# Kernel tuning notes

Hardware: AMD Instinct MI355X
Metric: run time of the kernel (lower is better)

## Reference

```python
import jax, jax.numpy as jnp
import numpy as np

N, D = 2, 256
M, L, K, DV = 8, 4, 4, 32
LK = L * K
LEVEL_HW = [(96, 96), (48, 48), (24, 24), (12, 12)]
S = sum(h * w for h, w in LEVEL_HW)  # 12240 flattened pyramid tokens
Q = S
OFFSET_SCALE = 0.5  # sampling_offset_scale_factor


def setup_inputs() -> dict:
    ks = jax.random.split(jax.random.key(0), 16)
    def lin(k, din, dout):
        return jax.random.normal(k, (din, dout), jnp.float32) / np.sqrt(din)
    return {
        "queries": jax.random.normal(ks[0], (N, Q, D), jnp.float32),
        "query_geometries": jax.random.uniform(ks[1], (N, Q, 4), jnp.float32, minval=0.1, maxval=0.9),
        "src_values": jax.random.normal(ks[2], (N, S, D), jnp.float32),
        "W_off": lin(ks[3], D, M * LK * 2) * 0.01,
        "b_off": jax.random.normal(ks[4], (M * LK * 2,), jnp.float32),
        "W_attn": lin(ks[5], D, M * LK),
        "b_attn": jnp.zeros((M * LK,), jnp.float32),
        "W_val": lin(ks[6], D, M * DV),
        "b_val": jnp.zeros((M * DV,), jnp.float32),
        "W_out": lin(ks[7], M * DV, D),
        "b_out": jnp.zeros((D,), jnp.float32),
    }


def _bilinear_sample(vmap_l, grid):
    # vmap_l: [B, dv, H, W]; grid: [B, Q, K, 2] in [-1, 1]
    # Matches F.grid_sample(mode='bilinear', align_corners=False, padding_mode='zeros')
    B, dv, H, W = vmap_l.shape
    x = (grid[..., 0] + 1.0) * (W / 2) - 0.5
    y = (grid[..., 1] + 1.0) * (H / 2) - 0.5
    x0 = jnp.floor(x)
    y0 = jnp.floor(y)
    wx = x - x0
    wy = y - y0
    x0i = x0.astype(jnp.int32)
    y0i = y0.astype(jnp.int32)
    vflat = vmap_l.reshape(B, dv, H * W)

    def corner(xi, yi, w):
        valid = (xi >= 0) & (xi < W) & (yi >= 0) & (yi < H)
        idx = jnp.clip(yi, 0, H - 1) * W + jnp.clip(xi, 0, W - 1)
        g = jax.vmap(lambda vf, i: vf[:, i])(vflat, idx)  # [B, dv, Q, K]
        return g * (w * valid)[:, None, :, :]

    return (corner(x0i, y0i, (1 - wx) * (1 - wy))
            + corner(x0i + 1, y0i, wx * (1 - wy))
            + corner(x0i, y0i + 1, (1 - wx) * wy)
            + corner(x0i + 1, y0i + 1, wx * wy))


def msdeform(queries, query_geometries, src_values, W_off, b_off, W_attn, b_attn,
             W_val, b_val, W_out, b_out):
    # attention weights: softmax over the L*K samples of each head
    attn = jax.nn.softmax((queries @ W_attn + b_attn).reshape(N, Q, M, LK), axis=-1)
    # predicted sampling offsets [N, Q, M, LK, 2]
    off = (queries @ W_off + b_off).reshape(N, Q, M, LK, 2)
    xy = query_geometries[..., :2]
    wh = query_geometries[..., 2:]
    scale = wh * (OFFSET_SCALE / K)  # wh * kv_count_per_level_inverse * sampling_offset_max_value
    pos = xy[:, :, None, None, :] + off * scale[:, :, None, None, :]  # normalized [0,1]
    # collapse (batch, head) -> B = N*M, rescale to [-1,1] for grid_sample semantics
    grid = (2.0 * pos - 1.0).transpose(0, 2, 1, 3, 4).reshape(N * M, Q, LK, 2)
    # project values and rebuild the per-level feature maps
    v = (src_values @ W_val + b_val).reshape(N, S, M, DV)
    samples, s = [], 0
    for l, (H, W) in enumerate(LEVEL_HW):
        vl = v[:, s:s + H * W].reshape(N, H, W, M, DV).transpose(0, 3, 4, 1, 2).reshape(N * M, DV, H, W)
        samples.append(_bilinear_sample(vl, grid[:, :, l * K:(l + 1) * K]))  # [N*M, DV, Q, K]
        s += H * W
    sampled = jnp.concatenate(samples, axis=-1)  # [N*M, DV, Q, LK]
    aw = attn.transpose(0, 2, 1, 3).reshape(N * M, 1, Q, LK)
    out = (sampled * aw).sum(-1)  # weighted reduction -> [N*M, DV, Q]
    out = out.reshape(N, M, DV, Q).transpose(0, 3, 1, 2).reshape(N, Q, M * DV)
    return out @ W_out + b_out  # backprojector


def reference(queries, query_geometries, src_values, W_off, b_off, W_attn, b_attn,
              W_val, b_val, W_out, b_out):
    return msdeform(queries, query_geometries, src_values, W_off, b_off, W_attn,
                    b_attn, W_val, b_val, W_out, b_out)
```

## Files before the change

kernel.cpp:

```cpp
#include <hip/hip_runtime.h>
#include <hip/hip_bf16.h>
#include <hip/hip_fp16.h>
#include <cstddef>

#define NB 2
#define QN 12240
#define SN 12240
#define MREAL 24480
#define MPAD  24576
#define MT    192

typedef unsigned short ushortT;
typedef unsigned int uintT;
typedef __bf16 bf16x8 __attribute__((ext_vector_type(8)));
typedef float f32x4 __attribute__((ext_vector_type(4)));

__device__ __forceinline__ ushortT f2bf(float f) {
    uintT u = __float_as_uint(f);
    uintT r = u + 0x7fffu + ((u >> 16) & 1u);
    return (ushortT)(r >> 16);
}
__device__ __forceinline__ float bf_lo(uintT u) {
    return __uint_as_float(u << 16);
}
__device__ __forceinline__ float bf_hi(uintT u) {
    return __uint_as_float(u & 0xffff0000u);
}

__device__ __forceinline__ void async_ld16(const ushortT* g, ushortT* l) {
    __builtin_amdgcn_global_load_lds(
        (const __attribute__((address_space(1))) unsigned int*)g,
        (__attribute__((address_space(3))) unsigned int*)l, 16, 0, 0);
}

__global__ __launch_bounds__(256) void cast_all(
    const float* __restrict__ q, const float* __restrict__ src,
    const float* __restrict__ Wval, const float* __restrict__ Wattn,
    const float* __restrict__ Woff, const float* __restrict__ Wout,
    ushortT* __restrict__ qb, ushortT* __restrict__ sb,
    ushortT* __restrict__ tval, ushortT* __restrict__ tlo,
    ushortT* __restrict__ tout)
{
    int bx = blockIdx.x;
    if (bx < 6120) {
        const int issrc = bx >= 3060;
        const size_t idx = ((size_t)(bx - (issrc ? 3060 : 0)) * 256 + threadIdx.x) * 8;
        const float* in = issrc ? src : q;
        ushortT* out = issrc ? sb : qb;
        const float4 a = *(const float4*)(in + idx);
        const float4 b = *(const float4*)(in + idx + 4);
        uint4 o;
        o.x = (uintT)f2bf(a.x) | ((uintT)f2bf(a.y) << 16);
        o.y = (uintT)f2bf(a.z) | ((uintT)f2bf(a.w) << 16);
        o.z = (uintT)f2bf(b.x) | ((uintT)f2bf(b.y) << 16);
        o.w = (uintT)f2bf(b.z) | ((uintT)f2bf(b.w) << 16);
        *(uint4*)(out + idx) = o;
        return;
    }
    bx -= 6120;
    const float* W; ushortT* T; int n, Nw, trow;
    if (bx < 256)      { W = Wval;  T = tval; n = bx;       Nw = 256; trow = n; }
    else if (bx < 384) { W = Wattn; T = tlo;  n = bx - 256; Nw = 128; trow = n; }
    else if (bx < 640) { W = Woff;  T = tlo;  n = bx - 384; Nw = 256; trow = n + 128; }
    else               { W = Wout;  T = tout; n = bx - 640; Nw = 256; trow = n; }
    const int k = threadIdx.x;
    T[(size_t)trow * 256 + k] = f2bf(W[(size_t)k * Nw + n]);
}

__global__ __launch_bounds__(256) void gemm_vlo(
    const ushortT* __restrict__ q_bf, const ushortT* __restrict__ src_bf,
    const ushortT* __restrict__ wt_val, const ushortT* __restrict__ wt_lo,
    const float* __restrict__ b_val, const float* __restrict__ b_attn,
    const float* __restrict__ b_off,
    ushortT* __restrict__ v_bf, float* __restrict__ lo_ws)
{
    const int z = blockIdx.x >= 2;
    const int col0 = (z ? blockIdx.x - 2 : blockIdx.x) * 128;

    __shared__ __attribute__((aligned(16))) ushortT As[128 * 32];
    __shared__ __attribute__((aligned(16))) ushortT Bs[128 * 32];

    const ushortT* A  = z ? q_bf : src_bf;
    const ushortT* Bt = z ? wt_lo : wt_val;

    const int tid  = threadIdx.x;
    const int wave = tid >> 6;
    const int lane = tid & 63;
    const int row0 = blockIdx.y * 128;
    const int wr = (wave >> 1) * 64;
    const int wc = (wave & 1) * 64;

    f32x4 acc[4][4];
    #pragma unroll
    for (int i = 0; i < 4; i++)
        #pragma unroll
        for (int j = 0; j < 4; j++)
            acc[i][j] = (f32x4)0.f;

    const int srow = (lane >> 2);
    const int sk8  = (lane & 3) * 8;

    for (int k0 = 0; k0 < 256; k0 += 32) {
        #pragma unroll
        for (int j = 0; j < 2; j++) {
            const int r = wave * 32 + j * 16;
            async_ld16(A  + (size_t)(row0 + r + srow) * 256 + k0 + sk8, &As[r * 32]);
            async_ld16(Bt + (size_t)(col0 + r + srow) * 256 + k0 + sk8, &Bs[r * 32]);
        }
        __syncthreads();

        bf16x8 af[4], bfr[4];
        const int mrow = lane & 15;
        const int kq   = (lane >> 4) * 8;
        #pragma unroll
        for (int i = 0; i < 4; i++) {
            af[i]  = *(const bf16x8*)&As[(wr + i * 16 + mrow) * 32 + kq];
            bfr[i] = *(const bf16x8*)&Bs[(wc + i * 16 + mrow) * 32 + kq];
        }
        #pragma unroll
        for (int i = 0; i < 4; i++)
            #pragma unroll
            for (int j = 0; j < 4; j++)
                acc[i][j] = __builtin_amdgcn_mfma_f32_16x16x32_bf16(
                    af[i], bfr[j], acc[i][j], 0, 0, 0);
        __syncthreads();
    }

    const float* bp = z ? ((col0 < 128) ? b_attn : b_off) : b_val;
    const int cofs  = (z && col0 >= 128) ? 128 : 0;

    #pragma unroll
    for (int i = 0; i < 4; i++) {
        const int rbase = row0 + wr + i * 16 + ((lane >> 4) << 2);
        #pragma unroll
        for (int j = 0; j < 4; j++) {
            const int col = col0 + wc + j * 16 + (lane & 15);
            const float bb = bp[col - cofs];
            #pragma unroll
            for (int r = 0; r < 4; r++) {
                const int row = rbase + r;
                if (row < MREAL) {
                    const float val = acc[i][j][r] + bb;
                    if (z) {
                        lo_ws[(size_t)row * 384 + col] = val;
                    } else {
                        const int nn = row / SN;
                        const int s  = row - nn * SN;
                        const int head = col >> 5, ch = col & 31;
                        v_bf[(((size_t)nn * 8 + head) * SN + s) * 32 + ch] = f2bf(val);
                    }
                }
            }
        }
    }
}

__global__ __launch_bounds__(256) void gemm_out(
    const ushortT* __restrict__ A, const ushortT* __restrict__ Bt,
    const float* __restrict__ bias, float* __restrict__ C)
{
    __shared__ __attribute__((aligned(16))) ushortT As[128 * 32];
    __shared__ __attribute__((aligned(16))) ushortT Bs[128 * 32];

    const int tid  = threadIdx.x;
    const int wave = tid >> 6;
    const int lane = tid & 63;
    const int row0 = blockIdx.y * 128;
    const int col0 = blockIdx.x * 128;
    const int wr = (wave >> 1) * 64;
    const int wc = (wave & 1) * 64;

    f32x4 acc[4][4];
    #pragma unroll
    for (int i = 0; i < 4; i++)
        #pragma unroll
        for (int j = 0; j < 4; j++)
            acc[i][j] = (f32x4)0.f;

    const int srow = (lane >> 2);
    const int sk8  = (lane & 3) * 8;

    for (int k0 = 0; k0 < 256; k0 += 32) {
        #pragma unroll
        for (int j = 0; j < 2; j++) {
            const int r = wave * 32 + j * 16;
            async_ld16(A  + (size_t)(row0 + r + srow) * 256 + k0 + sk8, &As[r * 32]);
            async_ld16(Bt + (size_t)(col0 + r + srow) * 256 + k0 + sk8, &Bs[r * 32]);
        }
        __syncthreads();

        bf16x8 af[4], bfr[4];
        const int mrow = lane & 15;
        const int kq   = (lane >> 4) * 8;
        #pragma unroll
        for (int i = 0; i < 4; i++) {
            af[i]  = *(const bf16x8*)&As[(wr + i * 16 + mrow) * 32 + kq];
            bfr[i] = *(const bf16x8*)&Bs[(wc + i * 16 + mrow) * 32 + kq];
        }
        #pragma unroll
        for (int i = 0; i < 4; i++)
            #pragma unroll
            for (int j = 0; j < 4; j++)
                acc[i][j] = __builtin_amdgcn_mfma_f32_16x16x32_bf16(
                    af[i], bfr[j], acc[i][j], 0, 0, 0);
        __syncthreads();
    }

    #pragma unroll
    for (int i = 0; i < 4; i++) {
        const int rbase = row0 + wr + i * 16 + ((lane >> 4) << 2);
        #pragma unroll
        for (int j = 0; j < 4; j++) {
            const int col = col0 + wc + j * 16 + (lane & 15);
            const float bb = bias[col];
            #pragma unroll
            for (int r = 0; r < 4; r++) {
                const int row = rbase + r;
                if (row < MREAL)
                    C[(size_t)row * 256 + col] = acc[i][j][r] + bb;
            }
        }
    }
}

__global__ __launch_bounds__(128) void sample_kernel(
    const float* __restrict__ lo,
    const float* __restrict__ geom,
    const ushortT* __restrict__ v,
    ushortT* __restrict__ out)
{
    const int tid  = threadIdx.x;
    const int w    = tid >> 6;
    const int lane = tid & 63;
    const int qi   = lane >> 3;
    const int m    = blockIdx.y;
    const int n    = blockIdx.z;
    const int q    = blockIdx.x * 16 + w * 8 + qi;

    __shared__ __attribute__((aligned(16))) int pls[2][544];

    const size_t qb = (size_t)n * QN + q;

    {
        const int p = lane & 7;
        const float* lorow = lo + qb * 384;
        const float2 lg = *(const float2*)(lorow + m * 16 + p * 2);
        const float4 of = *(const float4*)(lorow + 128 + m * 32 + p * 4);
        const float4 g  = *(const float4*)(geom + qb * 4);

        float mx = fmaxf(lg.x, lg.y);
        mx = fmaxf(mx, __shfl_xor(mx, 1));
        mx = fmaxf(mx, __shfl_xor(mx, 2));
        mx = fmaxf(mx, __shfl_xor(mx, 4));
        const float e0 = __expf(lg.x - mx);
        const float e1 = __expf(lg.y - mx);
        float s = e0 + e1;
        s += __shfl_xor(s, 1);
        s += __shfl_xor(s, 2);
        s += __shfl_xor(s, 4);
        const float inv = 1.f / s;

        const int l  = p >> 1;
        const int Wl = 96 >> l;
        const int s0 = (l == 0) ? 0 : (l == 1) ? 9216 : (l == 2) ? 11520 : 12096;
        const float cx = g.x, cy = g.y;
        const float sx = g.z * 0.125f, sy = g.w * 0.125f;
        int* myrec = &pls[w][qi * 68 + p * 8];

        #pragma unroll
        for (int t = 0; t < 2; t++) {
            const float ox = t ? of.z : of.x;
            const float oy = t ? of.w : of.y;
            const float wa = (t ? e1 : e0) * inv;

            const float x = (cx + ox * sx) * (float)Wl - 0.5f;
            const float y = (cy + oy * sy) * (float)Wl - 0.5f;
            const float xf = floorf(x), yf = floorf(y);
            const int x0 = (int)xf, y0 = (int)yf;
            const float wx = x - xf, wy = y - yf;

            const bool vx0 = (x0 >= 0) & (x0 < Wl);
            const bool vx1 = (x0 + 1 >= 0) & (x0 + 1 < Wl);
            const bool vy0 = (y0 >= 0) & (y0 < Wl);
            const bool vy1 = (y0 + 1 >= 0) & (y0 + 1 < Wl);

            const float w00 = (vx0 & vy0) ? wa * (1.f - wx) * (1.f - wy) : 0.f;
            const float w10 = (vx1 & vy0) ? wa * wx * (1.f - wy) : 0.f;
            const float w01 = (vx0 & vy1) ? wa * (1.f - wx) * wy : 0.f;
            const float w11 = (vx1 & vy1) ? wa * wx * wy : 0.f;

            const int xc0 = min(max(x0, 0), Wl - 1);
            const int xc1 = min(max(x0 + 1, 0), Wl - 1);
            const int yc0 = min(max(y0, 0), Wl - 1);
            const int yc1 = min(max(y0 + 1, 0), Wl - 1);

            const int iv0   = (s0 + yc0 * Wl + xc0) << 6;
            const int dx    = (xc1 - xc0) << 6;
            const int dyrow = ((yc1 - yc0) * Wl) << 6;
            __half2 h01 = __floats2half2_rn(w00, w10);
            __half2 h23 = __floats2half2_rn(w01, w11);
            int4 rec;
            rec.x = iv0;
            rec.y = dx | (dyrow << 16);
            rec.z = *reinterpret_cast<int*>(&h01);
            rec.w = *reinterpret_cast<int*>(&h23);
            *(int4*)(myrec + t * 4) = rec;
        }
    }
    __syncthreads();

    const int c = lane & 7;
    const unsigned char* vb = (const unsigned char*)
        (v + ((size_t)(n * 8 + m) * SN) * 32) + c * 8;
    const int* grec = &pls[w][qi * 68];

    float a0 = 0.f, a1 = 0.f, a2 = 0.f, a3 = 0.f;

    #pragma unroll
    for (int lk = 0; lk < 16; lk++) {
        const int4 rec = *(const int4*)(grec + lk * 4);
        const int base = rec.x;
        const int dx   = rec.y & 0xffff;
        const int dy   = ((uintT)rec.y) >> 16;

        const uint2 u0 = *(const uint2*)(vb + base);
        const uint2 u1 = *(const uint2*)(vb + base + dx);
        const uint2 u2 = *(const uint2*)(vb + base + dy);
        const uint2 u3 = *(const uint2*)(vb + base + dy + dx);

        const __half2 h01 = *reinterpret_cast<const __half2*>(&rec.z);
        const __half2 h23 = *reinterpret_cast<const __half2*>(&rec.w);
        const float2 wlo = __half22float2(h01);
        const float2 whi = __half22float2(h23);

        a0 += wlo.x * bf_lo(u0.x) + wlo.y * bf_lo(u1.x) + whi.x * bf_lo(u2.x) + whi.y * bf_lo(u3.x);
        a1 += wlo.x * bf_hi(u0.x) + wlo.y * bf_hi(u1.x) + whi.x * bf_hi(u2.x) + whi.y * bf_hi(u3.x);
        a2 += wlo.x * bf_lo(u0.y) + wlo.y * bf_lo(u1.y) + whi.x * bf_lo(u2.y) + whi.y * bf_lo(u3.y);
        a3 += wlo.x * bf_hi(u0.y) + wlo.y * bf_hi(u1.y) + whi.x * bf_hi(u2.y) + whi.y * bf_hi(u3.y);
    }

    ushort4 o;
    o.x = f2bf(a0); o.y = f2bf(a1); o.z = f2bf(a2); o.w = f2bf(a3);
    *(ushort4*)(out + qb * 256 + m * 32 + c * 4) = o;
}

extern "C" void kernel_launch(void* const* d_in, const int* in_sizes, int n_in,
                              void* d_out, int out_size, void* d_ws, size_t ws_size,
                              hipStream_t stream)
{
    const float* queries = (const float*)d_in[0];
    const float* geom    = (const float*)d_in[1];
    const float* src     = (const float*)d_in[2];
    const float* W_off   = (const float*)d_in[3];
    const float* b_off   = (const float*)d_in[4];
    const float* W_attn  = (const float*)d_in[5];
    const float* b_attn  = (const float*)d_in[6];
    const float* W_val   = (const float*)d_in[7];
    const float* b_val   = (const float*)d_in[8];
    const float* W_out   = (const float*)d_in[9];
    const float* b_out   = (const float*)d_in[10];
    float* out = (float*)d_out;

    ushortT* wsb = (ushortT*)d_ws;
    const size_t PADROW = (size_t)MPAD * 256;
    ushortT* q_bf    = wsb;
    ushortT* srcmdv  = wsb + PADROW;
    ushortT* v_bf    = wsb + 2 * PADROW;
    ushortT* wt_val  = wsb + 3 * PADROW;
    ushortT* wt_lo   = wt_val + 65536;
    ushortT* wt_out  = wt_lo + 98304;
    float* lo_ws = (float*)(wt_out + 65536);

    dim3 blk(256);

    cast_all<<<dim3(7016), blk, 0, stream>>>(
        queries, src, W_val, W_attn, W_off, W_out,
        q_bf, srcmdv, wt_val, wt_lo, wt_out);

    gemm_vlo<<<dim3(5, MT), blk, 0, stream>>>(
        q_bf, srcmdv, wt_val, wt_lo, b_val, b_attn, b_off, v_bf, lo_ws);

    sample_kernel<<<dim3(QN / 16, 8, NB), dim3(128), 0, stream>>>(
        lo_ws, geom, v_bf, srcmdv);

    gemm_out<<<dim3(2, MT), blk, 0, stream>>>(srcmdv, wt_out, b_out, out);
}
```

Before: 206.5 us.

## Hold weight fragments in registers and stream swizzled A panels through LDS

Both GEMM kernels are restructured. Each wave now preloads its full 256-deep weight slice as bf16 MFMA fragments in registers. Blocks of 512 threads stream 48-row A panels through a double-buffered, XOR-swizzled LDS buffer, 16 rows at a time. This removes the per-k-step reloading of B tiles and the two barriers per k-step of the old 128x128 tiling. In exchange it raises register pressure, and for the attention/offset projection the last column block computes 128 padding columns that are then discarded.

```diff
diff --git a/kernel.cpp b/kernel.cpp
--- a/kernel.cpp
+++ b/kernel.cpp
@@ -8,7 +8,6 @@
 #define SN 12240
 #define MREAL 24480
 #define MPAD  24576
-#define MT    192
 
 typedef unsigned short ushortT;
 typedef unsigned int uintT;
@@ -20,12 +19,8 @@
     uintT r = u + 0x7fffu + ((u >> 16) & 1u);
     return (ushortT)(r >> 16);
 }
-__device__ __forceinline__ float bf_lo(uintT u) {
-    return __uint_as_float(u << 16);
-}
-__device__ __forceinline__ float bf_hi(uintT u) {
-    return __uint_as_float(u & 0xffff0000u);
-}
+__device__ __forceinline__ float bf_lo(uintT u) { return __uint_as_float(u << 16); }
+__device__ __forceinline__ float bf_hi(uintT u) { return __uint_as_float(u & 0xffff0000u); }
 
 __device__ __forceinline__ void async_ld16(const ushortT* g, ushortT* l) {
     __builtin_amdgcn_global_load_lds(
@@ -67,158 +62,144 @@
     T[(size_t)trow * 256 + k] = f2bf(W[(size_t)k * Nw + n]);
 }
 
-__global__ __launch_bounds__(256) void gemm_vlo(
+__global__ __launch_bounds__(512, 4) void gemm_vlo(
     const ushortT* __restrict__ q_bf, const ushortT* __restrict__ src_bf,
     const ushortT* __restrict__ wt_val, const ushortT* __restrict__ wt_lo,
     const float* __restrict__ b_val, const float* __restrict__ b_attn,
     const float* __restrict__ b_off,
     ushortT* __restrict__ v_bf, float* __restrict__ lo_ws)
 {
-    const int z = blockIdx.x >= 2;
-    const int col0 = (z ? blockIdx.x - 2 : blockIdx.x) * 128;
-
-    __shared__ __attribute__((aligned(16))) ushortT As[128 * 32];
-    __shared__ __attribute__((aligned(16))) ushortT Bs[128 * 32];
-
-    const ushortT* A  = z ? q_bf : src_bf;
-    const ushortT* Bt = z ? wt_lo : wt_val;
-
-    const int tid  = threadIdx.x;
-    const int wave = tid >> 6;
-    const int lane = tid & 63;
-    const int row0 = blockIdx.y * 128;
-    const int wr = (wave >> 1) * 64;
-    const int wc = (wave & 1) * 64;
-
-    f32x4 acc[4][4];
+    const int bx = blockIdx.x;
+    const int tid = threadIdx.x, wave = tid >> 6, lane = tid & 63;
+    const bool isv = (bx == 0);
+    const ushortT* A  = isv ? src_bf : q_bf;
+    const ushortT* Bt = isv ? wt_val : wt_lo;
+    const int colbase = (isv ? 0 : (bx - 1) * 256) + wave * 32;
+
+    bf16x8 bfrag[8][2];
+    {
+        const int br = lane & 15, bk = (lane >> 4) * 8;
+        #pragma unroll
+        for (int k = 0; k < 8; k++)
+            #pragma unroll
+            for (int j = 0; j < 2; j++)
+                bfrag[k][j] = *(const bf16x8*)(
+                    Bt + (size_t)(colbase + j * 16 + br) * 256 + k * 32 + bk);
+    }
+
+    __shared__ __attribute__((aligned(16))) ushortT Apan[2][4096];
+
+    const int prow0 = blockIdx.y * 48;
+    const int sr = tid >> 5, sc = tid & 31;
+    const int sgc = sc ^ (sr & 7);
+
+    async_ld16(A + (size_t)(prow0 + sr) * 256 + sgc * 8, &Apan[0][tid * 8]);
+
+    const int rr = lane & 15, q4 = lane >> 4;
+
     #pragma unroll
-    for (int i = 0; i < 4; i++)
-        #pragma unroll
-        for (int j = 0; j < 4; j++)
-            acc[i][j] = (f32x4)0.f;
-
-    const int srow = (lane >> 2);
-    const int sk8  = (lane & 3) * 8;
-
-    for (int k0 = 0; k0 < 256; k0 += 32) {
-        #pragma unroll
-        for (int j = 0; j < 2; j++) {
-            const int r = wave * 32 + j * 16;
-            async_ld16(A  + (size_t)(row0 + r + srow) * 256 + k0 + sk8, &As[r * 32]);
-            async_ld16(Bt + (size_t)(col0 + r + srow) * 256 + k0 + sk8, &Bs[r * 32]);
-        }
+    for (int i = 0; i < 3; i++) {
         __syncthreads();
-
-        bf16x8 af[4], bfr[4];
-        const int mrow = lane & 15;
-        const int kq   = (lane >> 4) * 8;
-        #pragma unroll
-        for (int i = 0; i < 4; i++) {
-            af[i]  = *(const bf16x8*)&As[(wr + i * 16 + mrow) * 32 + kq];
-            bfr[i] = *(const bf16x8*)&Bs[(wc + i * 16 + mrow) * 32 + kq];
-        }
-        #pragma unroll
-        for (int i = 0; i < 4; i++)
-            #pragma unroll
-            for (int j = 0; j < 4; j++)
-                acc[i][j] = __builtin_amdgcn_mfma_f32_16x16x32_bf16(
-                    af[i], bfr[j], acc[i][j], 0, 0, 0);
-        __syncthreads();
-    }
-
-    const float* bp = z ? ((col0 < 128) ? b_attn : b_off) : b_val;
-    const int cofs  = (z && col0 >= 128) ? 128 : 0;
-
-    #pragma unroll
-    for (int i = 0; i < 4; i++) {
-        const int rbase = row0 + wr + i * 16 + ((lane >> 4) << 2);
-        #pragma unroll
-        for (int j = 0; j < 4; j++) {
-            const int col = col0 + wc + j * 16 + (lane & 15);
-            const float bb = bp[col - cofs];
-            #pragma unroll
-            for (int r = 0; r < 4; r++) {
-                const int row = rbase + r;
-                if (row < MREAL) {
-                    const float val = acc[i][j][r] + bb;
-                    if (z) {
-                        lo_ws[(size_t)row * 384 + col] = val;
-                    } else {
-                        const int nn = row / SN;
-                        const int s  = row - nn * SN;
-                        const int head = col >> 5, ch = col & 31;
-                        v_bf[(((size_t)nn * 8 + head) * SN + s) * 32 + ch] = f2bf(val);
-                    }
+        if (i < 2)
+            async_ld16(A + (size_t)(prow0 + (i + 1) * 16 + sr) * 256 + sgc * 8,
+                       &Apan[(i + 1) & 1][tid * 8]);
+
+        f32x4 acc0 = (f32x4)0.f, acc1 = (f32x4)0.f;
+        const ushortT* Ap = &Apan[i & 1][0];
+        #pragma unroll
+        for (int k = 0; k < 8; k++) {
+            const int p = (k * 4 + q4) ^ (rr & 7);
+            const bf16x8 af = *(const bf16x8*)(Ap + rr * 256 + p * 8);
+            acc0 = __builtin_amdgcn_mfma_f32_16x16x32_bf16(af, bfrag[k][0], acc0, 0, 0, 0);
+            acc1 = __builtin_amdgcn_mfma_f32_16x16x32_bf16(af, bfrag[k][1], acc1, 0, 0, 0);
+        }
+
+        const int rowb = prow0 + i * 16 + q4 * 4;
+        if (isv) {
+            #pragma unroll
+            for (int j = 0; j < 2; j++) {
+                const int col = colbase + j * 16 + rr;
+                const int head = col >> 5, ch = col & 31;
+                const f32x4 a = j ? acc1 : acc0;
+                const float bb = b_val[col];
+                #pragma unroll
+                for (int r = 0; r < 4; r++) {
+                    const int row = rowb + r;
+                    const int nn = (row >= SN) ? 1 : 0;
+                    const int s = row - nn * SN;
+                    v_bf[(((size_t)(nn * 8 + head)) * SN + s) * 32 + ch] = f2bf(a[r] + bb);
                 }
             }
-        }
-    }
-}
-
-__global__ __launch_bounds__(256) void gemm_out(
+        } else {
+            #pragma unroll
+            for (int j = 0; j < 2; j++) {
+                const int col = colbase + j * 16 + rr;
+                if (col < 384) {
+                    const float bb = (col < 128) ? b_attn[col] : b_off[col - 128];
+                    const f32x4 a = j ? acc1 : acc0;
+                    #pragma unroll
+                    for (int r = 0; r < 4; r++)
+                        lo_ws[(size_t)(rowb + r) * 384 + col] = a[r] + bb;
+                }
+            }
+        }
+    }
+}
+
+__global__ __launch_bounds__(512, 4) void gemm_out(
     const ushortT* __restrict__ A, const ushortT* __restrict__ Bt,
     const float* __restrict__ bias, float* __restrict__ C)
 {
-    __shared__ __attribute__((aligned(16))) ushortT As[128 * 32];
-    __shared__ __attribute__((aligned(16))) ushortT Bs[128 * 32];
-
-    const int tid  = threadIdx.x;
-    const int wave = tid >> 6;
-    const int lane = tid & 63;
-    const int row0 = blockIdx.y * 128;
-    const int col0 = blockIdx.x * 128;
-    const int wr = (wave >> 1) * 64;
-    const int wc = (wave & 1) * 64;
-
-    f32x4 acc[4][4];
+    const int tid = threadIdx.x, wave = tid >> 6, lane = tid & 63;
+    const int colbase = wave * 32;
+
+    bf16x8 bfrag[8][2];
+    {
+        const int br = lane & 15, bk = (lane >> 4) * 8;
+        #pragma unroll
+        for (int k = 0; k < 8; k++)
+            #pragma unroll
+            for (int j = 0; j < 2; j++)
+                bfrag[k][j] = *(const bf16x8*)(
+                    Bt + (size_t)(colbase + j * 16 + br) * 256 + k * 32 + bk);
+    }
+
+    __shared__ __attribute__((aligned(16))) ushortT Apan[2][4096];
+
+    const int prow0 = blockIdx.y * 48;
+    const int sr = tid >> 5, sc = tid & 31;
+    const int sgc = sc ^ (sr & 7);
+
+    async_ld16(A + (size_t)(prow0 + sr) * 256 + sgc * 8, &Apan[0][tid * 8]);
+
+    const int rr = lane & 15, q4 = lane >> 4;
+
     #pragma unroll
-    for (int i = 0; i < 4; i++)
-        #pragma unroll
-        for (int j = 0; j < 4; j++)
-            acc[i][j] = (f32x4)0.f;
-
-    const int srow = (lane >> 2);
-    const int sk8  = (lane & 3) * 8;
-
-    for (int k0 = 0; k0 < 256; k0 += 32) {
+    for (int i = 0; i < 3; i++) {
+        __syncthreads();
+        if (i < 2)
+            async_ld16(A + (size_t)(prow0 + (i + 1) * 16 + sr) * 256 + sgc * 8,
+                       &Apan[(i + 1) & 1][tid * 8]);
+
+        f32x4 acc0 = (f32x4)0.f, acc1 = (f32x4)0.f;
+        const ushortT* Ap = &Apan[i & 1][0];
+        #pragma unroll
+        for (int k = 0; k < 8; k++) {
+            const int p = (k * 4 + q4) ^ (rr & 7);
+            const bf16x8 af = *(const bf16x8*)(Ap + rr * 256 + p * 8);
+            acc0 = __builtin_amdgcn_mfma_f32_16x16x32_bf16(af, bfrag[k][0], acc0, 0, 0, 0);
+            acc1 = __builtin_amdgcn_mfma_f32_16x16x32_bf16(af, bfrag[k][1], acc1, 0, 0, 0);
+        }
+
+        const int rowb = prow0 + i * 16 + q4 * 4;
         #pragma unroll
         for (int j = 0; j < 2; j++) {
-            const int r = wave * 32 + j * 16;
-            async_ld16(A  + (size_t)(row0 + r + srow) * 256 + k0 + sk8, &As[r * 32]);
-            async_ld16(Bt + (size_t)(col0 + r + srow) * 256 + k0 + sk8, &Bs[r * 32]);
-        }
-        __syncthreads();
-
-        bf16x8 af[4], bfr[4];
-        const int mrow = lane & 15;
-        const int kq   = (lane >> 4) * 8;
-        #pragma unroll
-        for (int i = 0; i < 4; i++) {
-            af[i]  = *(const bf16x8*)&As[(wr + i * 16 + mrow) * 32 + kq];
-            bfr[i] = *(const bf16x8*)&Bs[(wc + i * 16 + mrow) * 32 + kq];
-        }
-        #pragma unroll
-        for (int i = 0; i < 4; i++)
-            #pragma unroll
-            for (int j = 0; j < 4; j++)
-                acc[i][j] = __builtin_amdgcn_mfma_f32_16x16x32_bf16(
-                    af[i], bfr[j], acc[i][j], 0, 0, 0);
-        __syncthreads();
-    }
-
-    #pragma unroll
-    for (int i = 0; i < 4; i++) {
-        const int rbase = row0 + wr + i * 16 + ((lane >> 4) << 2);
-        #pragma unroll
-        for (int j = 0; j < 4; j++) {
-            const int col = col0 + wc + j * 16 + (lane & 15);
+            const int col = colbase + j * 16 + rr;
             const float bb = bias[col];
-            #pragma unroll
-            for (int r = 0; r < 4; r++) {
-                const int row = rbase + r;
-                if (row < MREAL)
-                    C[(size_t)row * 256 + col] = acc[i][j][r] + bb;
-            }
+            const f32x4 a = j ? acc1 : acc0;
+            #pragma unroll
+            for (int r = 0; r < 4; r++)
+                C[(size_t)(rowb + r) * 256 + col] = a[r] + bb;
         }
     }
 }
@@ -368,20 +349,18 @@
     ushortT* v_bf    = wsb + 2 * PADROW;
     ushortT* wt_val  = wsb + 3 * PADROW;
     ushortT* wt_lo   = wt_val + 65536;
-    ushortT* wt_out  = wt_lo + 98304;
+    ushortT* wt_out  = wt_lo + 131072;
     float* lo_ws = (float*)(wt_out + 65536);
 
-    dim3 blk(256);
-
-    cast_all<<<dim3(7016), blk, 0, stream>>>(
+    cast_all<<<dim3(7016), dim3(256), 0, stream>>>(
         queries, src, W_val, W_attn, W_off, W_out,
         q_bf, srcmdv, wt_val, wt_lo, wt_out);
 
-    gemm_vlo<<<dim3(5, MT), blk, 0, stream>>>(
+    gemm_vlo<<<dim3(3, 510), dim3(512), 0, stream>>>(
         q_bf, srcmdv, wt_val, wt_lo, b_val, b_attn, b_off, v_bf, lo_ws);
 
     sample_kernel<<<dim3(QN / 16, 8, NB), dim3(128), 0, stream>>>(
         lo_ws, geom, v_bf, srcmdv);
 
-    gemm_out<<<dim3(2, MT), blk, 0, stream>>>(srcmdv, wt_out, b_out, out);
-}
+    gemm_out<<<dim3(1, 510), dim3(512), 0, stream>>>(srcmdv, wt_out, b_out, out);
+}
```

Measured after the change: 207.1 us. Within noise of the previous version (+0.3%).
